# Optimization experiments

Measured on AMD Instinct MI355X. Metric: run time of the kernel, lower is better.

The kernel has to match this reference:

```python
import jax, jax.numpy as jnp
import numpy as np

B, N, E = 4, 10000, 160000
D, H, HID, DE = 128, 4, 128, 16
DK = HID // H


def setup_inputs() -> dict:
    key = jax.random.key(0)
    ks = jax.random.split(key, 16)
    w = lambda k, shape: jax.random.normal(k, shape, jnp.float32) * 0.02
    return {
        "x": jax.random.normal(ks[0], (B, N, D), jnp.float32),
        "edge_index": jax.random.randint(ks[1], (2, E), 0, N, dtype=jnp.int32),
        "edge_attr": jax.random.normal(ks[2], (E, DE), jnp.float32),
        "Wq": w(ks[3], (D, HID)), "bq": jnp.zeros((HID,), jnp.float32),
        "Wk": w(ks[4], (D, HID)), "bk": jnp.zeros((HID,), jnp.float32),
        "Wv": w(ks[5], (D, HID)), "bv": jnp.zeros((HID,), jnp.float32),
        "Wf": w(ks[6], (DE, 2 * HID)), "bf": jnp.zeros((2 * HID,), jnp.float32),
        "Wo": w(ks[7], (HID, D)), "bo": jnp.zeros((D,), jnp.float32),
        "ln_g": jnp.ones((D,), jnp.float32), "ln_b": jnp.zeros((D,), jnp.float32),
    }


def reference(x, edge_index, edge_attr, Wq, bq, Wk, bk, Wv, bv, Wf, bf, Wo, bo, ln_g, ln_b):
    src, dst = edge_index[0], edge_index[1]
    # node projections -> [B, N, H, DK]
    Q = (x @ Wq + bq).reshape(B, N, H, DK)
    K = (x @ Wk + bk).reshape(B, N, H, DK)
    V = (x @ Wv + bv).reshape(B, N, H, DK)
    # edge gathers -> [B, E, H, DK]
    q_e, k_e, v_e = Q[:, dst], K[:, src], V[:, src]
    # FiLM modulation of keys (edge-conditioned, shared across batch)
    gamma, beta = jnp.split(edge_attr @ Wf + bf, 2, axis=-1)
    gamma = gamma.reshape(1, E, H, DK)
    beta = beta.reshape(1, E, H, DK)
    k_e = k_e * (1.0 + gamma) + beta
    logits = (q_e * k_e).sum(-1) / np.sqrt(DK).astype(np.float32)  # [B, E, H]

    def seg_softmax(lg):  # lg: [E, H], softmax over edges sharing a dst node
        m = jax.ops.segment_max(lg, dst, num_segments=N)       # [N, H]
        ex = jnp.exp(lg - m[dst])
        s = jax.ops.segment_sum(ex, dst, num_segments=N)        # [N, H]
        return ex / s[dst]

    att = jax.vmap(seg_softmax)(logits)                         # [B, E, H]
    msg = att[..., None] * v_e                                  # [B, E, H, DK]
    agg = jax.vmap(lambda m: jax.ops.segment_sum(m, dst, num_segments=N))(msg)
    y = agg.reshape(B, N, HID) @ Wo + bo                        # [B, N, D]
    h = x + y  # dropout is identity in eval mode
    mu = h.mean(-1, keepdims=True)
    var = ((h - mu) ** 2).mean(-1, keepdims=True)
    return (h - mu) / jnp.sqrt(var + 1e-5) * ln_g + ln_b
```

## Files before the change

kernel.cpp:

```cpp
#include <hip/hip_runtime.h>
#include <hip/hip_bf16.h>

#define B_ 4
#define N_ 10000
#define E_ 160000
#define D_ 128
#define H_ 4
#define HID_ 128
#define DK_ 32
#define DE_ 16
#define PGRID 2048

typedef __attribute__((ext_vector_type(8))) short short8v;
typedef __attribute__((ext_vector_type(4))) short short4v;
typedef __attribute__((ext_vector_type(4))) float f32x4;
typedef __attribute__((ext_vector_type(2))) float f32x2;

__device__ __forceinline__ short bfb(float f) {
  union { float f; unsigned u; } c; c.f = f;
  unsigned u = c.u + 0x7FFFu + ((c.u >> 16) & 1u);
  return (short)(u >> 16);
}
__device__ __forceinline__ float b2f(unsigned short u) {
  union { unsigned u; float f; } c; c.u = ((unsigned)u) << 16;
  return c.f;
}

__device__ __forceinline__ unsigned char f2fp8(float f) {
  int r = __builtin_amdgcn_cvt_pk_fp8_f32(f, f, 0, false);
  return (unsigned char)(r & 0xff);
}
__device__ __forceinline__ f32x2 fp8lo(unsigned u) {
  return __builtin_amdgcn_cvt_pk_f32_fp8((int)u, false);
}
__device__ __forceinline__ f32x2 fp8hi(unsigned u) {
  return __builtin_amdgcn_cvt_pk_f32_fp8((int)u, true);
}

__global__ __launch_bounds__(256) void wt_prep(
    const float* __restrict__ Wq, const float* __restrict__ Wk,
    const float* __restrict__ Wv, const float* __restrict__ Wo,
    short* __restrict__ wt) {
  const float* Ws[4] = {Wq, Wk, Wv, Wo};
  const int i = blockIdx.x * 256 + threadIdx.x;
  const int m = i >> 14;
  const int k = (i >> 7) & 127;
  const int n = i & 127;
  wt[(size_t)m * 16384 + n * 128 + k] = bfb(Ws[m][k * 128 + n]);
}

__global__ __launch_bounds__(64) void qkv_mfma(
    const float* __restrict__ x, const short* __restrict__ wt,
    const float* __restrict__ bq, const float* __restrict__ bk,
    const float* __restrict__ bv,
    unsigned short* __restrict__ Qb, unsigned char* __restrict__ kv8) {
  __shared__ short xs[16][136];
  const int lane = threadIdx.x;
  const int ln15 = lane & 15;
  const int g    = lane >> 4;
  const long rowBase = (long)blockIdx.x * 16;

  for (int i = lane; i < 16 * 32; i += 64) {
    const int r  = i >> 5;
    const int c4 = (i & 31) * 4;
    const float4 v = *(const float4*)(x + (rowBase + r) * 128 + c4);
    short4v sv; sv.x = bfb(v.x); sv.y = bfb(v.y); sv.z = bfb(v.z); sv.w = bfb(v.w);
    *(short4v*)&xs[r][c4] = sv;
  }
  __syncthreads();

  short8v af[4];
#pragma unroll
  for (int kk = 0; kk < 4; ++kk)
    af[kk] = *(const short8v*)&xs[ln15][kk * 32 + g * 8];

  const float* bs[3] = {bq, bk, bv};

  int bbv[4], nnv[4];
#pragma unroll
  for (int r = 0; r < 4; ++r) {
    const long row = rowBase + g * 4 + r;
    bbv[r] = (int)(row / N_);
    nnv[r] = (int)(row - (long)bbv[r] * N_);
  }

#pragma unroll
  for (int m = 0; m < 3; ++m) {
    const short* Wt = wt + (size_t)m * 16384;
    f32x4 acc[8];
#pragma unroll
    for (int cb = 0; cb < 8; ++cb) acc[cb] = (f32x4){0.f, 0.f, 0.f, 0.f};

#pragma unroll
    for (int kk = 0; kk < 4; ++kk) {
#pragma unroll
      for (int cb = 0; cb < 8; ++cb) {
        const short8v bfr =
            *(const short8v*)(Wt + (cb * 16 + ln15) * 128 + kk * 32 + g * 8);
        acc[cb] = __builtin_amdgcn_mfma_f32_16x16x32_bf16(af[kk], bfr, acc[cb], 0, 0, 0);
      }
    }

    const float* bias = bs[m];
#pragma unroll
    for (int cb = 0; cb < 8; ++cb) {
      const int col = cb * 16 + ln15;
      const float bv_ = bias[col];
#pragma unroll
      for (int r = 0; r < 4; ++r) {
        const float val = acc[cb][r] + bv_;
        if (m == 0) {
          const long row = rowBase + g * 4 + r;
          Qb[row * 128 + col] = (unsigned short)bfb(val);
        } else {
          kv8[(((size_t)nnv[r] * 4 + bbv[r]) << 8) + (m - 1) * 128 + col] = f2fp8(val);
        }
      }
    }
  }
}

__global__ __launch_bounds__(256) void csr_hist(const int* __restrict__ ei,
                                                int* __restrict__ cnt) {
  const int e = blockIdx.x * 256 + threadIdx.x;
  if (e < E_) atomicAdd(&cnt[ei[E_ + e]], 1);
}

__global__ __launch_bounds__(1024) void csr_scan(const int* __restrict__ cnt,
                                                 int* __restrict__ rowptr,
                                                 int* __restrict__ fill) {
  __shared__ int part[1024];
  const int t = threadIdx.x;
  int local[10];
  int sum = 0;
#pragma unroll
  for (int i = 0; i < 10; ++i) {
    const int idx = t * 10 + i;
    local[i] = sum;
    sum += (idx < N_) ? cnt[idx] : 0;
  }
  part[t] = sum;
  __syncthreads();
  for (int off = 1; off < 1024; off <<= 1) {
    const int v = (t >= off) ? part[t - off] : 0;
    __syncthreads();
    part[t] += v;
    __syncthreads();
  }
  const int excl = (t == 0) ? 0 : part[t - 1];
#pragma unroll
  for (int i = 0; i < 10; ++i) {
    const int idx = t * 10 + i;
    if (idx <= N_) {
      const int o = excl + local[i];
      rowptr[idx] = o;
      if (idx < N_) fill[idx] = o;
    }
  }
}

__global__ __launch_bounds__(256) void csr_scatter(
    const int* __restrict__ ei, const float* __restrict__ ea,
    int* __restrict__ fill, int* __restrict__ esrc, float* __restrict__ eas) {
  const int e = blockIdx.x * 256 + threadIdx.x;
  if (e < E_) {
    const int dst = ei[E_ + e];
    const int pos = atomicAdd(&fill[dst], 1);
    esrc[pos] = ei[e];
    const float4* s4 = (const float4*)(ea + (size_t)e * 16);
    float4* d4 = (float4*)(eas + (size_t)pos * 16);
    d4[0] = s4[0]; d4[1] = s4[1]; d4[2] = s4[2]; d4[3] = s4[3];
  }
}

__global__ __launch_bounds__(256) void film_prep(
    const float* __restrict__ eas, const float* __restrict__ Wf,
    const float* __restrict__ bf, unsigned char* __restrict__ film8) {
  const int lane = threadIdx.x & 63;
  const int wave = threadIdx.x >> 6;
  const int c0 = lane * 4;

  float4 w[16];
#pragma unroll
  for (int j = 0; j < 16; ++j) w[j] = *(const float4*)(Wf + j * 256 + c0);
  const float4 bias = *(const float4*)(bf + c0);

  for (int i = blockIdx.x * 4 + wave; i < E_; i += PGRID * 4) {
    const float* ep = eas + (size_t)i * 16;
    const float4 a0 = *(const float4*)ep;
    const float4 a1 = *(const float4*)(ep + 4);
    const float4 a2 = *(const float4*)(ep + 8);
    const float4 a3 = *(const float4*)(ep + 12);
    const float ev[16] = {a0.x,a0.y,a0.z,a0.w, a1.x,a1.y,a1.z,a1.w,
                          a2.x,a2.y,a2.z,a2.w, a3.x,a3.y,a3.z,a3.w};
    float ox = bias.x, oy = bias.y, oz = bias.z, ow = bias.w;
#pragma unroll
    for (int j = 0; j < 16; ++j) {
      ox = fmaf(ev[j], w[j].x, ox);
      oy = fmaf(ev[j], w[j].y, oy);
      oz = fmaf(ev[j], w[j].z, oz);
      ow = fmaf(ev[j], w[j].w, ow);
    }
    int r = __builtin_amdgcn_cvt_pk_fp8_f32(ox, oy, 0, false);
    r = __builtin_amdgcn_cvt_pk_fp8_f32(oz, ow, r, true);
    ((int*)(film8 + (size_t)i * 256))[lane] = r;
  }
}

__global__ __launch_bounds__(256) void fused_attn(
    const int* __restrict__ rowptr, const int* __restrict__ esrc,
    const unsigned char* __restrict__ film8, const unsigned short* __restrict__ Qb,
    const unsigned char* __restrict__ kv8, float* __restrict__ agg) {
  const int wave = threadIdx.x >> 6;
  const int lane = threadIdx.x & 63;
  const int e2 = lane >> 5;
  const int dh = (lane >> 4) & 1;
  const int b  = (lane >> 2) & 3;
  const int h  = lane & 3;
  const int col0 = h * 32 + dh * 16;

  for (int node = blockIdx.x * 4 + wave; node < N_; node += PGRID * 4) {
    const int beg = rowptr[node], end = rowptr[node + 1];

    float q[16];
    {
      const unsigned short* qp = Qb + ((size_t)b * N_ + node) * 128 + col0;
      const short8v t0 = *(const short8v*)qp;
      const short8v t1 = *(const short8v*)(qp + 8);
#pragma unroll
      for (int j = 0; j < 8; ++j) {
        q[j]     = b2f((unsigned short)t0[j]);
        q[8 + j] = b2f((unsigned short)t1[j]);
      }
    }
    float acc[16];
#pragma unroll
    for (int d = 0; d < 16; ++d) acc[d] = 0.f;
    float se = 0.f;

    for (int i0 = beg; i0 < end; i0 += 2) {
      const int ii = i0 + e2;
      const bool valid = ii < end;
      const int ic = valid ? ii : i0;
      const int src = esrc[ic];
      const unsigned char* kp = kv8 + ((((size_t)src << 2) + b) << 8) + col0;
      const unsigned char* fp = film8 + (size_t)ic * 256 + col0;
      const uint4 kw = *(const uint4*)kp;
      const uint4 vw = *(const uint4*)(kp + 128);
      const uint4 gw = *(const uint4*)fp;
      const uint4 tw = *(const uint4*)(fp + 128);
      const unsigned ks[4] = {kw.x, kw.y, kw.z, kw.w};
      const unsigned vs[4] = {vw.x, vw.y, vw.z, vw.w};
      const unsigned gs[4] = {gw.x, gw.y, gw.z, gw.w};
      const unsigned ts[4] = {tw.x, tw.y, tw.z, tw.w};

      float pacc[4] = {0.f, 0.f, 0.f, 0.f};
#pragma unroll
      for (int w = 0; w < 4; ++w) {
        const f32x2 k0 = fp8lo(ks[w]), k1 = fp8hi(ks[w]);
        const f32x2 g0 = fp8lo(gs[w]), g1 = fp8hi(gs[w]);
        const f32x2 t0 = fp8lo(ts[w]), t1 = fp8hi(ts[w]);
        float km;
        km = k0.x + fmaf(k0.x, g0.x, t0.x); pacc[w] = fmaf(q[4*w+0], km, pacc[w]);
        km = k0.y + fmaf(k0.y, g0.y, t0.y); pacc[w] = fmaf(q[4*w+1], km, pacc[w]);
        km = k1.x + fmaf(k1.x, g1.x, t1.x); pacc[w] = fmaf(q[4*w+2], km, pacc[w]);
        km = k1.y + fmaf(k1.y, g1.y, t1.y); pacc[w] = fmaf(q[4*w+3], km, pacc[w]);
      }
      float pl = (pacc[0] + pacc[1]) + (pacc[2] + pacc[3]);
      pl += __shfl_xor(pl, 16);

      float ex = __expf(pl * 0.17677669529663687f);
      ex = valid ? ex : 0.f;
      se += ex;
#pragma unroll
      for (int w = 0; w < 4; ++w) {
        const f32x2 v0 = fp8lo(vs[w]), v1 = fp8hi(vs[w]);
        acc[4*w+0] = fmaf(ex, v0.x, acc[4*w+0]);
        acc[4*w+1] = fmaf(ex, v0.y, acc[4*w+1]);
        acc[4*w+2] = fmaf(ex, v1.x, acc[4*w+2]);
        acc[4*w+3] = fmaf(ex, v1.y, acc[4*w+3]);
      }
    }

#pragma unroll
    for (int d = 0; d < 16; ++d) acc[d] += __shfl_xor(acc[d], 32);
    se += __shfl_xor(se, 32);

    if (e2 == 0) {
      const float inv = (end > beg) ? 1.f / se : 0.f;
      float* ap = agg + ((size_t)b * N_ + node) * 128 + col0;
#pragma unroll
      for (int c = 0; c < 4; ++c) {
        float4 o;
        o.x = acc[c*4+0] * inv; o.y = acc[c*4+1] * inv;
        o.z = acc[c*4+2] * inv; o.w = acc[c*4+3] * inv;
        *(float4*)(ap + c * 4) = o;
      }
    }
  }
}

__global__ __launch_bounds__(64) void out_ln_mfma(
    const float* __restrict__ agg, const short* __restrict__ wto,
    const float* __restrict__ bo, const float* __restrict__ x,
    const float* __restrict__ lng, const float* __restrict__ lnb,
    float* __restrict__ out) {
  __shared__ short as_[16][136];
  const int lane = threadIdx.x;
  const int ln15 = lane & 15;
  const int g    = lane >> 4;
  const long rowBase = (long)blockIdx.x * 16;

  for (int i = lane; i < 16 * 32; i += 64) {
    const int r  = i >> 5;
    const int c4 = (i & 31) * 4;
    const float4 v = *(const float4*)(agg + (rowBase + r) * 128 + c4);
    short4v sv; sv.x = bfb(v.x); sv.y = bfb(v.y); sv.z = bfb(v.z); sv.w = bfb(v.w);
    *(short4v*)&as_[r][c4] = sv;
  }
  __syncthreads();

  short8v af[4];
#pragma unroll
  for (int kk = 0; kk < 4; ++kk)
    af[kk] = *(const short8v*)&as_[ln15][kk * 32 + g * 8];

  f32x4 acc[8];
#pragma unroll
  for (int cb = 0; cb < 8; ++cb) acc[cb] = (f32x4){0.f, 0.f, 0.f, 0.f};

#pragma unroll
  for (int kk = 0; kk < 4; ++kk) {
#pragma unroll
    for (int cb = 0; cb < 8; ++cb) {
      const short8v bfr =
          *(const short8v*)(wto + (cb * 16 + ln15) * 128 + kk * 32 + g * 8);
      acc[cb] = __builtin_amdgcn_mfma_f32_16x16x32_bf16(af[kk], bfr, acc[cb], 0, 0, 0);
    }
  }

#pragma unroll
  for (int cb = 0; cb < 8; ++cb) {
    const int col = cb * 16 + ln15;
    const float bov = bo[col];
#pragma unroll
    for (int r = 0; r < 4; ++r) {
      const long row = rowBase + g * 4 + r;
      acc[cb][r] += bov + x[row * 128 + col];
    }
  }

  float s1[4], s2[4];
#pragma unroll
  for (int r = 0; r < 4; ++r) {
    s1[r] = 0.f; s2[r] = 0.f;
#pragma unroll
    for (int cb = 0; cb < 8; ++cb) {
      s1[r] += acc[cb][r];
      s2[r] = fmaf(acc[cb][r], acc[cb][r], s2[r]);
    }
  }
#pragma unroll
  for (int m = 1; m < 16; m <<= 1) {
#pragma unroll
    for (int r = 0; r < 4; ++r) {
      s1[r] += __shfl_xor(s1[r], m);
      s2[r] += __shfl_xor(s2[r], m);
    }
  }
  float mu[4], inv[4];
#pragma unroll
  for (int r = 0; r < 4; ++r) {
    mu[r] = s1[r] * (1.f / 128.f);
    const float var = s2[r] * (1.f / 128.f) - mu[r] * mu[r];
    inv[r] = rsqrtf(var + 1e-5f);
  }

#pragma unroll
  for (int cb = 0; cb < 8; ++cb) {
    const int col = cb * 16 + ln15;
    const float gv = lng[col], bv_ = lnb[col];
#pragma unroll
    for (int r = 0; r < 4; ++r) {
      const long row = rowBase + g * 4 + r;
      out[row * 128 + col] = (acc[cb][r] - mu[r]) * inv[r] * gv + bv_;
    }
  }
}

extern "C" void kernel_launch(void* const* d_in, const int* in_sizes, int n_in,
                              void* d_out, int out_size, void* d_ws, size_t ws_size,
                              hipStream_t stream) {
  const float* x   = (const float*)d_in[0];
  const int*   ei  = (const int*)d_in[1];
  const float* ea  = (const float*)d_in[2];
  const float* Wq  = (const float*)d_in[3];
  const float* bq  = (const float*)d_in[4];
  const float* Wk  = (const float*)d_in[5];
  const float* bk  = (const float*)d_in[6];
  const float* Wv  = (const float*)d_in[7];
  const float* bv  = (const float*)d_in[8];
  const float* Wf  = (const float*)d_in[9];
  const float* bf  = (const float*)d_in[10];
  const float* Wo  = (const float*)d_in[11];
  const float* bo  = (const float*)d_in[12];
  const float* lng = (const float*)d_in[13];
  const float* lnb = (const float*)d_in[14];
  float* out = (float*)d_out;

  const size_t NQ = (size_t)B_ * N_ * HID_;

  char* base = (char*)d_ws;
  size_t off = 0;
  unsigned short* Qb = (unsigned short*)(base + off); off += NQ * 2;
  float* agg  = (float*)(base + off); off += NQ * 4;
  float* eas  = (float*)(base + off); off += (size_t)E_ * 16 * 4;
  unsigned char* kv8 = (unsigned char*)(base + off);
  off += (size_t)B_ * N_ * 256;
  unsigned char* film8 = (unsigned char*)(base + off);
  off += (size_t)E_ * 256;
  short* wt   = (short*)(base + off); off += 4 * 16384 * 2;
  int*  cnt    = (int*)(base + off); off += N_ * 4;
  int*  rowptr = (int*)(base + off); off += (N_ + 1) * 4;
  int*  fill   = (int*)(base + off); off += N_ * 4;
  int*  esrc   = (int*)(base + off); off += E_ * 4;

  hipMemsetAsync(cnt, 0, N_ * sizeof(int), stream);

  wt_prep<<<256, 256, 0, stream>>>(Wq, Wk, Wv, Wo, wt);
  qkv_mfma<<<(B_ * N_) / 16, 64, 0, stream>>>(x, wt, bq, bk, bv, Qb, kv8);
  csr_hist<<<(E_ + 255) / 256, 256, 0, stream>>>(ei, cnt);
  csr_scan<<<1, 1024, 0, stream>>>(cnt, rowptr, fill);
  csr_scatter<<<(E_ + 255) / 256, 256, 0, stream>>>(ei, ea, fill, esrc, eas);
  film_prep<<<PGRID, 256, 0, stream>>>(eas, Wf, bf, film8);
  fused_attn<<<PGRID, 256, 0, stream>>>(rowptr, esrc, film8, Qb, kv8, agg);
  out_ln_mfma<<<(B_ * N_) / 16, 64, 0, stream>>>(agg, wt + 3 * 16384, bo, x, lng, lnb, out);
}
```

Measured before the change: 173.2 us.

## Merge weight prep with CSR histogram; index FiLM by original edge order

Folds the weight transpose/bf16 conversion and the destination histogram into one launch, removing a kernel launch. The CSR scatter no longer copies the 64-byte edge attributes into sorted order. It records the original edge id instead, so film_prep reads edge_attr directly and fused_attn looks up FiLM rows through that permutation. This saves a scatter pass and a buffer, at the cost of an extra index load and non-contiguous FiLM reads in the attention loop.

```diff
diff --git a/kernel.cpp b/kernel.cpp
--- a/kernel.cpp
+++ b/kernel.cpp
@@ -37,16 +37,23 @@
   return __builtin_amdgcn_cvt_pk_f32_fp8((int)u, true);
 }
 
-__global__ __launch_bounds__(256) void wt_prep(
+__global__ __launch_bounds__(256) void wt_hist(
     const float* __restrict__ Wq, const float* __restrict__ Wk,
     const float* __restrict__ Wv, const float* __restrict__ Wo,
-    short* __restrict__ wt) {
-  const float* Ws[4] = {Wq, Wk, Wv, Wo};
-  const int i = blockIdx.x * 256 + threadIdx.x;
-  const int m = i >> 14;
-  const int k = (i >> 7) & 127;
-  const int n = i & 127;
-  wt[(size_t)m * 16384 + n * 128 + k] = bfb(Ws[m][k * 128 + n]);
+    short* __restrict__ wt, const int* __restrict__ ei,
+    int* __restrict__ cnt) {
+  const int blk = blockIdx.x;
+  if (blk < 256) {
+    const float* Ws[4] = {Wq, Wk, Wv, Wo};
+    const int i = blk * 256 + threadIdx.x;
+    const int m = i >> 14;
+    const int k = (i >> 7) & 127;
+    const int n = i & 127;
+    wt[(size_t)m * 16384 + n * 128 + k] = bfb(Ws[m][k * 128 + n]);
+  } else {
+    const int e = (blk - 256) * 256 + threadIdx.x;
+    if (e < E_) atomicAdd(&cnt[ei[E_ + e]], 1);
+  }
 }
 
 __global__ __launch_bounds__(64) void qkv_mfma(
@@ -120,12 +127,6 @@
   }
 }
 
-__global__ __launch_bounds__(256) void csr_hist(const int* __restrict__ ei,
-                                                int* __restrict__ cnt) {
-  const int e = blockIdx.x * 256 + threadIdx.x;
-  if (e < E_) atomicAdd(&cnt[ei[E_ + e]], 1);
-}
-
 __global__ __launch_bounds__(1024) void csr_scan(const int* __restrict__ cnt,
                                                  int* __restrict__ rowptr,
                                                  int* __restrict__ fill) {
@@ -160,21 +161,19 @@
 }
 
 __global__ __launch_bounds__(256) void csr_scatter(
-    const int* __restrict__ ei, const float* __restrict__ ea,
-    int* __restrict__ fill, int* __restrict__ esrc, float* __restrict__ eas) {
+    const int* __restrict__ ei, int* __restrict__ fill,
+    int* __restrict__ esrc, int* __restrict__ eord) {
   const int e = blockIdx.x * 256 + threadIdx.x;
   if (e < E_) {
     const int dst = ei[E_ + e];
     const int pos = atomicAdd(&fill[dst], 1);
     esrc[pos] = ei[e];
-    const float4* s4 = (const float4*)(ea + (size_t)e * 16);
-    float4* d4 = (float4*)(eas + (size_t)pos * 16);
-    d4[0] = s4[0]; d4[1] = s4[1]; d4[2] = s4[2]; d4[3] = s4[3];
+    eord[pos] = e;
   }
 }
 
 __global__ __launch_bounds__(256) void film_prep(
-    const float* __restrict__ eas, const float* __restrict__ Wf,
+    const float* __restrict__ ea, const float* __restrict__ Wf,
     const float* __restrict__ bf, unsigned char* __restrict__ film8) {
   const int lane = threadIdx.x & 63;
   const int wave = threadIdx.x >> 6;
@@ -186,7 +185,7 @@
   const float4 bias = *(const float4*)(bf + c0);
 
   for (int i = blockIdx.x * 4 + wave; i < E_; i += PGRID * 4) {
-    const float* ep = eas + (size_t)i * 16;
+    const float* ep = ea + (size_t)i * 16;
     const float4 a0 = *(const float4*)ep;
     const float4 a1 = *(const float4*)(ep + 4);
     const float4 a2 = *(const float4*)(ep + 8);
@@ -209,7 +208,8 @@
 
 __global__ __launch_bounds__(256) void fused_attn(
     const int* __restrict__ rowptr, const int* __restrict__ esrc,
-    const unsigned char* __restrict__ film8, const unsigned short* __restrict__ Qb,
+    const int* __restrict__ eord, const unsigned char* __restrict__ film8,
+    const unsigned short* __restrict__ Qb,
     const unsigned char* __restrict__ kv8, float* __restrict__ agg) {
   const int wave = threadIdx.x >> 6;
   const int lane = threadIdx.x & 63;
@@ -243,8 +243,9 @@
       const bool valid = ii < end;
       const int ic = valid ? ii : i0;
       const int src = esrc[ic];
+      const int de  = eord[ic];
       const unsigned char* kp = kv8 + ((((size_t)src << 2) + b) << 8) + col0;
-      const unsigned char* fp = film8 + (size_t)ic * 256 + col0;
+      const unsigned char* fp = film8 + (size_t)de * 256 + col0;
       const uint4 kw = *(const uint4*)kp;
       const uint4 vw = *(const uint4*)(kp + 128);
       const uint4 gw = *(const uint4*)fp;
@@ -414,7 +415,6 @@
   size_t off = 0;
   unsigned short* Qb = (unsigned short*)(base + off); off += NQ * 2;
   float* agg  = (float*)(base + off); off += NQ * 4;
-  float* eas  = (float*)(base + off); off += (size_t)E_ * 16 * 4;
   unsigned char* kv8 = (unsigned char*)(base + off);
   off += (size_t)B_ * N_ * 256;
   unsigned char* film8 = (unsigned char*)(base + off);
@@ -424,15 +424,15 @@
   int*  rowptr = (int*)(base + off); off += (N_ + 1) * 4;
   int*  fill   = (int*)(base + off); off += N_ * 4;
   int*  esrc   = (int*)(base + off); off += E_ * 4;
+  int*  eord   = (int*)(base + off); off += E_ * 4;
 
   hipMemsetAsync(cnt, 0, N_ * sizeof(int), stream);
 
-  wt_prep<<<256, 256, 0, stream>>>(Wq, Wk, Wv, Wo, wt);
+  wt_hist<<<256 + (E_ + 255) / 256, 256, 0, stream>>>(Wq, Wk, Wv, Wo, wt, ei, cnt);
   qkv_mfma<<<(B_ * N_) / 16, 64, 0, stream>>>(x, wt, bq, bk, bv, Qb, kv8);
-  csr_hist<<<(E_ + 255) / 256, 256, 0, stream>>>(ei, cnt);
   csr_scan<<<1, 1024, 0, stream>>>(cnt, rowptr, fill);
-  csr_scatter<<<(E_ + 255) / 256, 256, 0, stream>>>(ei, ea, fill, esrc, eas);
-  film_prep<<<PGRID, 256, 0, stream>>>(eas, Wf, bf, film8);
-  fused_attn<<<PGRID, 256, 0, stream>>>(rowptr, esrc, film8, Qb, kv8, agg);
+  csr_scatter<<<(E_ + 255) / 256, 256, 0, stream>>>(ei, fill, esrc, eord);
+  film_prep<<<PGRID, 256, 0, stream>>>(ea, Wf, bf, film8);
+  fused_attn<<<PGRID, 256, 0, stream>>>(rowptr, esrc, eord, film8, Qb, kv8, agg);
   out_ln_mfma<<<(B_ * N_) / 16, 64, 0, stream>>>(agg, wt + 3 * 16384, bo, x, lng, lnb, out);
 }
```

Result: no change. 171.5 us (-1.0%).
